# Optimization experiments

Hardware: AMD Instinct MI355X
Metric: run time of the kernel (lower is better)

The kernel has to match this reference:

```python
import jax, jax.numpy as jnp
import numpy as np

N, E, C, L, G, O = 100000, 1600000, 128, 7, 2, 40
BETA = 0.9
HEADS, HC = 1, 128  # heads=1, head_channels=hidden_channels=128


def setup_inputs() -> dict:
    key = jax.random.key(0)
    ks = jax.random.split(key, 16)
    s = 0.05  # ~ torch Linear init std for fan_in=128
    inp = {
        'x': jax.random.normal(ks[0], (N, C), jnp.float32),
        'edge_index': jax.random.randint(ks[1], (2, E), 0, N, jnp.int64),
        'Wh': jax.random.normal(ks[2], (L, C, C)) * s,
        'bh': jax.random.normal(ks[3], (L, C)) * s,
        'Wg': jax.random.normal(ks[4], (L, C, C)) * s,
        'bg': jax.random.normal(ks[5], (L, C)) * s,
        'Wl': jax.random.normal(ks[6], (L, C, C)) * s,
        'bl': jax.random.normal(ks[7], (L, C)) * s,
        'ln_g': jnp.ones((L, C)), 'ln_b': jnp.zeros((L, C)),
        'bn_g': jnp.ones((L, C)), 'bn_b': jnp.zeros((L, C)),
        'bn_rm': jnp.zeros((L, C)), 'bn_rv': jnp.ones((L, C)),
        'gWh': jax.random.normal(ks[8], (G, C, C)) * s,
        'gbh': jax.random.normal(ks[9], (G, C)) * s,
        'gWk': jax.random.normal(ks[10], (G, C, C)) * s,
        'gWv': jax.random.normal(ks[11], (G, C, C)) * s,
        'gln_g': jnp.ones((G, C)), 'gln_b': jnp.zeros((G, C)),
        'gWo': jax.random.normal(ks[12], (G, C, C)) * s,
        'gbo': jax.random.normal(ks[13], (G, C)) * s,
        'f_ln_g': jnp.ones((C,)), 'f_ln_b': jnp.zeros((C,)),
        'Wp': jax.random.normal(ks[14], (O, C)) * s,
        'bp': jax.random.normal(ks[15], (O,)) * s,
    }
    return inp


def _layer_norm(x, g, b, eps=1e-5):
    mu = jnp.mean(x, axis=-1, keepdims=True)
    var = jnp.mean((x - mu) ** 2, axis=-1, keepdims=True)
    return (x - mu) * jax.lax.rsqrt(var + eps) * g + b


def reference(x, edge_index, Wh, bh, Wg, bg, Wl, bl, ln_g, ln_b,
              bn_g, bn_b, bn_rm, bn_rv, gWh, gbh, gWk, gWv,
              gln_g, gln_b, gWo, gbo, f_ln_g, f_ln_b, Wp, bp):
    n = x.shape[0]
    src, dst = edge_index[0], edge_index[1]
    # gcn_norm with add_self_loops=True: deg over destination incl. self loop
    deg = jnp.zeros((n,), x.dtype).at[dst].add(1.0) + 1.0
    dinv = jax.lax.rsqrt(deg)
    enorm = (dinv[src] * dinv[dst])[:, None]   # [E,1]
    selfw = (dinv * dinv)[:, None]             # [N,1] self-loop weight

    x_local = jnp.zeros_like(x @ Wh[0].T)
    for i in range(L):
        h = jax.nn.relu(x @ Wh[i].T + bh[i])
        xw = x @ Wg[i].T                                  # GCN lin (bias separate)
        agg = jax.ops.segment_sum(xw[src] * enorm, dst, num_segments=n)
        conv = agg + xw * selfw + bg[i]
        x = conv + x @ Wl[i].T + bl[i]
        # BatchNorm1d in eval mode (running stats)
        x = (x - bn_rm[i]) * jax.lax.rsqrt(bn_rv[i] + 1e-5) * bn_g[i] + bn_b[i]
        x = jax.nn.relu(x)
        x = (1.0 - BETA) * _layer_norm(h * x, ln_g[i], ln_b[i]) + BETA * x
        x_local = x_local + x

    # global linear attention (PolynormerAttention, qk_shared=True, qkv_bias=False)
    xg = _layer_norm(x_local, f_ln_g, f_ln_b)
    for j in range(G):
        h = xg @ gWh[j].T + gbh[j]
        k = jax.nn.sigmoid(xg @ gWk[j].T).reshape(n, HEADS, HC)
        q = k
        v = (xg @ gWv[j].T).reshape(n, HEADS, HC)
        kv = jnp.einsum('ndh,ndm->dhm', k, v)            # [heads,hc,hc]
        num = jnp.einsum('ndh,dhm->ndm', q, kv)          # [N,heads,hc]
        k_sum = jnp.sum(k, axis=0)                       # [heads,hc]
        den = jnp.einsum('ndh,dh->nd', q, k_sum)[..., None]
        attn = (num / (den + 1e-6)).reshape(n, HEADS * HC)
        xg = _layer_norm(attn, gln_g[j], gln_b[j]) * (h + BETA)
        xg = jax.nn.relu(xg @ gWo[j].T + gbo[j])

    return xg @ Wp.T + bp
```

## Files before the change

### kernel.cpp

```cpp
#include <hip/hip_runtime.h>

typedef unsigned short u16;
typedef unsigned int u32;
typedef __attribute__((ext_vector_type(8))) short short8;
typedef __attribute__((ext_vector_type(8))) unsigned short ushort8v;
typedef __attribute__((ext_vector_type(4))) float f32x4;

#define CDIM 128

__device__ __forceinline__ float b2f(u16 u){ return __uint_as_float(((unsigned)u)<<16); }
__device__ __forceinline__ u16 f2b(float f){
  unsigned x = __float_as_uint(f);
  unsigned r = (x + 0x7fffu + ((x>>16)&1u)) >> 16;
  return (u16)r;
}
__device__ __forceinline__ float wsum64(float v){
  #pragma unroll
  for(int d=1; d<64; d<<=1) v += __shfl_xor(v, d, 64);
  return v;
}
__device__ __forceinline__ float wsum16(float v){
  v += __shfl_xor(v, 1, 64);
  v += __shfl_xor(v, 2, 64);
  v += __shfl_xor(v, 4, 64);
  v += __shfl_xor(v, 8, 64);
  return v;
}

__global__ void k_probe(const u32* __restrict__ x, const u32* __restrict__ ei, int* __restrict__ flags){
  __shared__ int s_bf, s_nz;
  if(threadIdx.x == 0){ s_bf = 0; s_nz = 0; }
  __syncthreads();
  int c_bf = 0, c_nz = 0;
  for(int i = threadIdx.x; i < 4096; i += 256){
    u32 w = x[i];
    u32 e = (w >> 7) & 0xFFu;
    if(e >= 100u && e <= 140u) c_bf++;
    if(ei[2*i + 1] != 0u) c_nz++;
  }
  atomicAdd(&s_bf, c_bf);
  atomicAdd(&s_nz, c_nz);
  __syncthreads();
  if(threadIdx.x == 0){
    flags[0] = (s_bf < 2048) ? 1 : 0;
    flags[1] = (s_nz < 8) ? 1 : 0;
  }
}

__global__ void k_cvt_x(const void* __restrict__ src, u16* __restrict__ dst, int n,
                        const int* __restrict__ flags){
  int i = (blockIdx.x*256 + threadIdx.x)*8;
  if(i + 7 >= n) return;
  if(flags[0]){
    const float* s = (const float*)src + i;
    float4 a = *(const float4*)s;
    float4 b = *(const float4*)(s + 4);
    ushort8v o;
    o[0]=f2b(a.x); o[1]=f2b(a.y); o[2]=f2b(a.z); o[3]=f2b(a.w);
    o[4]=f2b(b.x); o[5]=f2b(b.y); o[6]=f2b(b.z); o[7]=f2b(b.w);
    *(ushort8v*)(dst + i) = o;
  } else {
    *(ushort8v*)(dst + i) = *(const ushort8v*)((const u16*)src + i);
  }
}

struct CvtArgs {
  const void* src[24];
  u16* dst[24];
  int n[24];
};

__global__ void k_cvt_params(CvtArgs a, const int* __restrict__ flags){
  int seg = blockIdx.y;
  int i = blockIdx.x*256 + threadIdx.x;
  int n = a.n[seg];
  if(i >= n) return;
  if(flags[0]) a.dst[seg][i] = f2b(((const float*)a.src[seg])[i]);
  else         a.dst[seg][i] = ((const u16*)a.src[seg])[i];
}

__global__ void k_cvt_ei_count(const int* __restrict__ src, int* __restrict__ dst, int E,
                               const int* __restrict__ flags, u32* __restrict__ cnt){
  int i = blockIdx.x*256 + threadIdx.x;
  if(i >= 2*E) return;
  int v = flags[1] ? src[2*i] : src[i];
  dst[i] = v;
  if(i >= E) atomicAdd(&cnt[v], 1u);
}

__global__ __launch_bounds__(256) void k_scan1(const u32* __restrict__ cnt, int n, u32* __restrict__ bsum){
  const int lane = threadIdx.x & 63;
  const int wv = threadIdx.x >> 6;
  int i = blockIdx.x*256 + threadIdx.x;
  u32 v = (i < n) ? cnt[i] : 0u;
  #pragma unroll
  for(int d=1; d<64; d<<=1) v += (u32)__shfl_xor((int)v, d, 64);
  __shared__ u32 ws[4];
  if(lane == 0) ws[wv] = v;
  __syncthreads();
  if(threadIdx.x == 0) bsum[blockIdx.x] = ws[0] + ws[1] + ws[2] + ws[3];
}

__global__ __launch_bounds__(1024) void k_scan2(const u32* __restrict__ bsum, int nb, u32* __restrict__ bpre){
  __shared__ u32 s[1024];
  int t = threadIdx.x;
  u32 v = (t < nb) ? bsum[t] : 0u;
  s[t] = v;
  __syncthreads();
  for(int d=1; d<1024; d<<=1){
    u32 y = (t >= d) ? s[t-d] : 0u;
    __syncthreads();
    s[t] += y;
    __syncthreads();
  }
  if(t < nb) bpre[t] = s[t] - v;
}

__global__ __launch_bounds__(256) void k_scan3(const u32* __restrict__ cnt, int n,
                                               const u32* __restrict__ bpre,
                                               u32* __restrict__ rowstart, u32* __restrict__ cursor,
                                               float* __restrict__ dinv){
  const int lane = threadIdx.x & 63;
  const int wv = threadIdx.x >> 6;
  int i = blockIdx.x*256 + threadIdx.x;
  u32 v = (i < n) ? cnt[i] : 0u;
  u32 x = v;
  #pragma unroll
  for(int d=1; d<64; d<<=1){
    u32 y = (u32)__shfl_up((int)x, d, 64);
    if(lane >= d) x += y;
  }
  __shared__ u32 ws[4];
  if(lane == 63) ws[wv] = x;
  __syncthreads();
  u32 woff = 0;
  #pragma unroll
  for(int w=0; w<4; w++) if(w < wv) woff += ws[w];
  u32 incl = x + woff;
  u32 rs = bpre[blockIdx.x] + incl - v;
  if(i < n){
    rowstart[i] = rs;
    cursor[i] = rs;
    dinv[i] = rsqrtf((float)(v + 1u));
    if(i == n-1) rowstart[n] = rs + v;
  }
}

__global__ __launch_bounds__(256) void k_scatter8(
  const int* __restrict__ ei, int E, int Nn, int nsl,
  u32* __restrict__ cursor, const float* __restrict__ dinv, int2* __restrict__ colw)
{
  const int r = blockIdx.x & 7;
  const int slice = blockIdx.x >> 3;
  const int q = (Nn + 7) >> 3;
  const int lo = r*q;
  const int hi = (lo + q < Nn) ? lo + q : Nn;
  const int chunk = (E + nsl - 1) / nsl;
  int e0 = slice*chunk;
  int e1 = e0 + chunk; if(e1 > E) e1 = E;
  for(int e = e0 + threadIdx.x; e < e1; e += 256){
    int d = ei[E + e];
    if(d >= lo && d < hi){
      int s = ei[e];
      u32 p = atomicAdd(&cursor[d], 1u);
      colw[p] = make_int2(s, __float_as_int(dinv[s]));
    }
  }
}

__global__ __launch_bounds__(256) void k_gemm3(
  const u16* __restrict__ A, int M,
  const u16* __restrict__ W0, const u16* __restrict__ bs0, int op0, u16* __restrict__ O0,
  const u16* __restrict__ W1, const u16* __restrict__ bs1, int op1, u16* __restrict__ O1,
  const u16* __restrict__ W2, const u16* __restrict__ bs2, int op2, u16* __restrict__ O2)
{
  __shared__ u16 stg[4][32*136];
  const int lane = threadIdx.x & 63;
  const int wv = threadIdx.x >> 6;
  const int l16 = lane & 15, quad = lane >> 4;
  const long nbase = (long)blockIdx.x*128 + wv*32;

  const u16* Ws[3] = {W0, W1, W2};
  const u16* Bs[3] = {bs0, bs1, bs2};
  u16* Os[3] = {O0, O1, O2};
  const int ops[3] = {op0, op1, op2};
  const int w = blockIdx.y;
  const u16* Wm = Ws[w];
  const int op = ops[w];
  u16* Op = Os[w];
  const u16* bp = Bs[w];
  u16* st = stg[wv];

  short8 xf[2][4];
  #pragma unroll
  for(int nt=0; nt<2; nt++){
    long r = nbase + nt*16 + l16; if(r >= M) r = M-1;
    const u16* ap = A + r*CDIM + quad*8;
    #pragma unroll
    for(int kt=0; kt<4; kt++)
      xf[nt][kt] = *(const short8*)(ap + kt*32);
  }

  #pragma unroll
  for(int ct=0; ct<8; ct++){
    f32x4 acc0 = {0.f,0.f,0.f,0.f}, acc1 = {0.f,0.f,0.f,0.f};
    const u16* wp = Wm + (ct*16 + l16)*CDIM + quad*8;
    #pragma unroll
    for(int kt=0; kt<4; kt++){
      short8 wf = *(const short8*)(wp + kt*32);
      acc0 = __builtin_amdgcn_mfma_f32_16x16x32_bf16(wf, xf[0][kt], acc0, 0, 0, 0);
      acc1 = __builtin_amdgcn_mfma_f32_16x16x32_bf16(wf, xf[1][kt], acc1, 0, 0, 0);
    }
    float bv[4] = {0.f,0.f,0.f,0.f};
    if(bp){
      ushort4 bq = *(const ushort4*)(bp + ct*16 + quad*4);
      bv[0]=b2f(bq.x); bv[1]=b2f(bq.y); bv[2]=b2f(bq.z); bv[3]=b2f(bq.w);
    }
    #pragma unroll
    for(int nt=0; nt<2; nt++){
      f32x4 a = nt ? acc1 : acc0;
      u16 o[4];
      #pragma unroll
      for(int g=0; g<4; g++){
        float v = a[g] + bv[g];
        if(op == 1) v = fmaxf(v, 0.f);
        else if(op == 2) v = 1.f/(1.f + __expf(-v));
        o[g] = f2b(v);
      }
      u32 p0 = (u32)o[0] | ((u32)o[1] << 16);
      u32 p1 = (u32)o[2] | ((u32)o[3] << 16);
      *(uint2*)&st[(nt*16 + l16)*136 + ct*16 + quad*4] = make_uint2(p0, p1);
    }
  }
  #pragma unroll
  for(int p2=0; p2<8; p2++){
    int row = (p2>>2)*16 + (lane>>2);
    int seg = (lane&3) + (p2&3)*4;
    long node = nbase + row;
    ushort8v v = *(const ushort8v*)&st[row*136 + seg*8];
    if(node < M)
      *(ushort8v*)(Op + (size_t)node*CDIM + seg*8) = v;
  }
}

__global__ __launch_bounds__(256) void k_layer_epi(
  const u16* __restrict__ xw, const u16* __restrict__ h, const u16* __restrict__ xl,
  const int2* __restrict__ colw, const u32* __restrict__ rowstart, const float* __restrict__ dinv,
  const u16* __restrict__ bg, const u16* __restrict__ bng, const u16* __restrict__ bnb,
  const u16* __restrict__ bnrm, const u16* __restrict__ bnrv,
  const u16* __restrict__ lng, const u16* __restrict__ lnb,
  const u16* __restrict__ flng, const u16* __restrict__ flnb,
  float* __restrict__ xlocal, u16* __restrict__ xout, int n, int first, int final)
{
  __shared__ float redis[4][128];
  const int lane = threadIdx.x & 63;
  const int quad = lane >> 4;
  const int l16 = lane & 15;
  const int wv = threadIdx.x >> 6;
  int node = blockIdx.x*4 + wv;
  const int valid = (node < n);
  if(!valid) node = n - 1;
  const int cg = l16*8;
  u32 j0 = rowstart[node], j1 = rowstart[node+1];
  float a[8];
  #pragma unroll
  for(int g=0; g<8; g++) a[g] = 0.f;

  for(u32 base = j0; base < j1; base += 64){
    int avail = (int)(j1 - base);
    int cnt = avail < 64 ? avail : 64;
    int2 pw = make_int2(0, 0);
    if(lane < cnt) pw = colw[base + lane];
    int cntp = (cnt + 15) & ~15;
    for(int t = 0; t < cntp; t += 16){
      int s[4]; float w[4]; ushort8v v[4];
      #pragma unroll
      for(int u=0; u<4; u++){
        s[u] = __shfl(pw.x, t + u*4 + quad, 64);
        w[u] = __int_as_float(__shfl(pw.y, t + u*4 + quad, 64));
      }
      #pragma unroll
      for(int u=0; u<4; u++) v[u] = *(const ushort8v*)(xw + (size_t)s[u]*CDIM + cg);
      #pragma unroll
      for(int u=0; u<4; u++){
        #pragma unroll
        for(int g=0; g<8; g++) a[g] = fmaf(w[u], b2f(v[u][g]), a[g]);
      }
    }
  }
  #pragma unroll
  for(int g=0; g<8; g++){
    a[g] += __shfl_xor(a[g], 16, 64);
    a[g] += __shfl_xor(a[g], 32, 64);
  }
  if(quad == 0){
    *(float4*)&redis[wv][cg]     = make_float4(a[0],a[1],a[2],a[3]);
    *(float4*)&redis[wv][cg + 4] = make_float4(a[4],a[5],a[6],a[7]);
  }
  __syncthreads();
  const int c0 = lane*2;
  float2 av = *(float2*)&redis[wv][c0];
  float a0 = av.x, a1 = av.y;

  float dn = dinv[node], sw = dn*dn;
  size_t base = (size_t)node*CDIM + c0;
  ushort2 xwv = *(const ushort2*)(xw + base);
  ushort2 xlv = *(const ushort2*)(xl + base);
  ushort2 hv  = *(const ushort2*)(h  + base);
  float x10 = a0*dn + b2f(xwv.x)*sw + b2f(bg[c0])   + b2f(xlv.x);
  float x11 = a1*dn + b2f(xwv.y)*sw + b2f(bg[c0+1]) + b2f(xlv.y);
  float s0 = rsqrtf(b2f(bnrv[c0])   + 1e-5f) * b2f(bng[c0]);
  float s1 = rsqrtf(b2f(bnrv[c0+1]) + 1e-5f) * b2f(bng[c0+1]);
  float x20 = (x10 - b2f(bnrm[c0]))*s0   + b2f(bnb[c0]);
  float x21 = (x11 - b2f(bnrm[c0+1]))*s1 + b2f(bnb[c0+1]);
  float x30 = fmaxf(x20, 0.f);
  float x31 = fmaxf(x21, 0.f);
  float t0 = b2f(hv.x)*x30, t1 = b2f(hv.y)*x31;
  float mu = wsum64(t0 + t1) * (1.f/128.f);
  float d0 = t0 - mu, d1 = t1 - mu;
  float var = wsum64(d0*d0 + d1*d1) * (1.f/128.f);
  float inv = rsqrtf(var + 1e-5f);
  float y0 = d0*inv*b2f(lng[c0])   + b2f(lnb[c0]);
  float y1 = d1*inv*b2f(lng[c0+1]) + b2f(lnb[c0+1]);
  float xn0 = 0.1f*y0 + 0.9f*x30;
  float xn1 = 0.1f*y1 + 0.9f*x31;
  float2 xl2;
  if(first){
    xl2.x = xn0; xl2.y = xn1;
  } else {
    xl2 = *(float2*)(xlocal + base);
    xl2.x += xn0; xl2.y += xn1;
  }
  if(!final){
    if(valid){
      *(float2*)(xlocal + base) = xl2;
      ushort2 o; o.x = f2b(xn0); o.y = f2b(xn1);
      *(ushort2*)(xout + base) = o;
    }
  } else {
    float mu2 = wsum64(xl2.x + xl2.y) * (1.f/128.f);
    float e0 = xl2.x - mu2, e1 = xl2.y - mu2;
    float var2 = wsum64(e0*e0 + e1*e1) * (1.f/128.f);
    float inv2 = rsqrtf(var2 + 1e-5f);
    if(valid){
      ushort2 o;
      o.x = f2b(e0*inv2*b2f(flng[c0])   + b2f(flnb[c0]));
      o.y = f2b(e1*inv2*b2f(flng[c0+1]) + b2f(flnb[c0+1]));
      *(ushort2*)(xout + base) = o;
    }
  }
}

__global__ __launch_bounds__(256) void k_kv(
  const u16* __restrict__ kk, const u16* __restrict__ vv, int n, int npb,
  float* __restrict__ part)
{
  __shared__ float sk[8][128];
  __shared__ float sv[8][128];
  const int tid = threadIdx.x;
  const int tr = tid >> 4, tc = tid & 15;
  float acc[8][8];
  #pragma unroll
  for(int i=0;i<8;i++){
    #pragma unroll
    for(int j=0;j<8;j++) acc[i][j] = 0.f;
  }
  float ks[8];
  #pragma unroll
  for(int i=0;i<8;i++) ks[i] = 0.f;
  int start = blockIdx.x * npb;
  int end = start + npb; if(end > n) end = n;
  const int lr = tid >> 5;
  const int lc = (tid & 31) * 4;
  for(int g0 = start; g0 < end; g0 += 8){
    int cnt = end - g0; if(cnt > 8) cnt = 8;
    __syncthreads();
    if(lr < cnt){
      ushort4 kq = *(const ushort4*)(kk + (size_t)(g0+lr)*CDIM + lc);
      ushort4 vq = *(const ushort4*)(vv + (size_t)(g0+lr)*CDIM + lc);
      sk[lr][lc] = b2f(kq.x); sk[lr][lc+1] = b2f(kq.y); sk[lr][lc+2] = b2f(kq.z); sk[lr][lc+3] = b2f(kq.w);
      sv[lr][lc] = b2f(vq.x); sv[lr][lc+1] = b2f(vq.y); sv[lr][lc+2] = b2f(vq.z); sv[lr][lc+3] = b2f(vq.w);
    }
    __syncthreads();
    for(int r=0; r<cnt; r++){
      float4 ka = *(const float4*)&sk[r][tr*8];
      float4 kb = *(const float4*)&sk[r][tr*8+4];
      float4 va = *(const float4*)&sv[r][tc*8];
      float4 vb = *(const float4*)&sv[r][tc*8+4];
      float kr[8] = {ka.x,ka.y,ka.z,ka.w,kb.x,kb.y,kb.z,kb.w};
      float vr[8] = {va.x,va.y,va.z,va.w,vb.x,vb.y,vb.z,vb.w};
      #pragma unroll
      for(int i=0;i<8;i++){
        #pragma unroll
        for(int j=0;j<8;j++) acc[i][j] = fmaf(kr[i], vr[j], acc[i][j]);
      }
      if(tc == 0){
        #pragma unroll
        for(int i=0;i<8;i++) ks[i] += kr[i];
      }
    }
  }
  float* p = part + (size_t)blockIdx.x * 16512;
  #pragma unroll
  for(int i=0;i<8;i++){
    #pragma unroll
    for(int j=0;j<8;j++)
      p[(size_t)(tc*8+j)*CDIM + tr*8 + i] = acc[i][j];
  }
  if(tc == 0){
    #pragma unroll
    for(int i=0;i<8;i++) p[16384 + tr*8 + i] = ks[i];
  }
}

__global__ void k_kvred(const float* __restrict__ part, int nb, u16* __restrict__ Bext){
  int i = blockIdx.x*256 + threadIdx.x;
  if(i >= 144*128) return;
  float s = 0.f;
  if(i < 16512){
    #pragma unroll 8
    for(int b=0;b<nb;b++) s += part[(size_t)b*16512 + i];
  }
  Bext[i] = f2b(s);
}

__global__ __launch_bounds__(256) void k_attn(
  const u16* __restrict__ q, const u16* __restrict__ Bext, const u16* __restrict__ hg,
  const u16* __restrict__ g, const u16* __restrict__ b,
  u16* __restrict__ out, int M)
{
  __shared__ u16 stg[4][32*136];
  const int lane = threadIdx.x & 63;
  const int wv = threadIdx.x >> 6;
  const int l16 = lane & 15, quad = lane >> 4;
  const long rbase = (long)blockIdx.x*128 + wv*32;
  u16* st = stg[wv];

  short8 af[2][4];
  #pragma unroll
  for(int rt=0; rt<2; rt++){
    long r = rbase + rt*16 + l16; if(r >= M) r = M-1;
    const u16* ap = q + r*CDIM + quad*8;
    #pragma unroll
    for(int kt=0; kt<4; kt++)
      af[rt][kt] = *(const short8*)(ap + kt*32);
  }
  f32x4 acc[2][9];
  f32x4 zero = {0.f,0.f,0.f,0.f};
  #pragma unroll
  for(int rt=0; rt<2; rt++){
    #pragma unroll
    for(int ct=0; ct<9; ct++) acc[rt][ct] = zero;
  }
  #pragma unroll
  for(int ct=0; ct<9; ct++){
    const u16* wp = Bext + (ct*16 + l16)*CDIM + quad*8;
    #pragma unroll
    for(int kt=0; kt<4; kt++){
      short8 bf = *(const short8*)(wp + kt*32);
      acc[0][ct] = __builtin_amdgcn_mfma_f32_16x16x32_bf16(af[0][kt], bf, acc[0][ct], 0, 0, 0);
      acc[1][ct] = __builtin_amdgcn_mfma_f32_16x16x32_bf16(af[1][kt], bf, acc[1][ct], 0, 0, 0);
    }
  }
  #pragma unroll
  for(int rt=0; rt<2; rt++){
    float rden[4];
    #pragma unroll
    for(int gi=0; gi<4; gi++){
      float dv = __shfl(acc[rt][8][gi], lane & 48, 64);
      rden[gi] = 1.f/(dv + 1e-6f);
    }
    #pragma unroll
    for(int gi=0; gi<4; gi++){
      float sum = 0.f;
      #pragma unroll
      for(int ct=0; ct<8; ct++) sum += acc[rt][ct][gi]*rden[gi];
      float mu = wsum16(sum) * (1.f/128.f);
      float vs = 0.f;
      #pragma unroll
      for(int ct=0; ct<8; ct++){ float d = acc[rt][ct][gi]*rden[gi] - mu; vs = fmaf(d, d, vs); }
      float inv = rsqrtf(wsum16(vs)*(1.f/128.f) + 1e-5f);
      const int rowl = rt*16 + quad*4 + gi;
      #pragma unroll
      for(int ct=0; ct<8; ct++){
        int col = ct*16 + l16;
        float y = (acc[rt][ct][gi]*rden[gi] - mu)*inv*b2f(g[col]) + b2f(b[col]);
        st[rowl*136 + col] = f2b(y);
      }
    }
  }
  #pragma unroll
  for(int p2=0; p2<8; p2++){
    int row = (p2>>2)*16 + (lane>>2);
    int seg = (lane&3) + (p2&3)*4;
    long node = rbase + row;
    if(node >= M) node = M-1;
    ushort8v yv = *(const ushort8v*)&st[row*136 + seg*8];
    ushort8v hv = *(const ushort8v*)(hg + (size_t)node*CDIM + seg*8);
    ushort8v o;
    #pragma unroll
    for(int i2=0; i2<8; i2++)
      o[i2] = f2b(b2f(yv[i2]) * (b2f(hv[i2]) + 0.9f));
    if(rbase + row < M)
      *(ushort8v*)(out + (size_t)node*CDIM + seg*8) = o;
  }
}

__global__ __launch_bounds__(256) void k_gout(
  const u16* __restrict__ A, const u16* __restrict__ W, const u16* __restrict__ bs,
  void* __restrict__ outv, int M, const int* __restrict__ flags)
{
  const int lane = threadIdx.x & 63;
  const int wv = threadIdx.x >> 6;
  const int l16 = lane & 15, quad = lane >> 4;
  const long rbase = (long)blockIdx.x*128 + wv*32;
  const int f32m = flags[0];
  short8 af[2][4];
  #pragma unroll
  for(int rt=0; rt<2; rt++){
    long r = rbase + rt*16 + l16; if(r >= M) r = M-1;
    const u16* ap = A + r*CDIM + quad*8;
    #pragma unroll
    for(int kt=0; kt<4; kt++)
      af[rt][kt] = *(const short8*)(ap + kt*32);
  }
  f32x4 acc[2][3];
  f32x4 zero = {0.f,0.f,0.f,0.f};
  #pragma unroll
  for(int rt=0; rt<2; rt++){
    #pragma unroll
    for(int ct=0; ct<3; ct++) acc[rt][ct] = zero;
  }
  #pragma unroll
  for(int ct=0; ct<3; ct++){
    int row = ct*16 + l16; if(row > 39) row = 39;
    const u16* wp = W + row*CDIM + quad*8;
    #pragma unroll
    for(int kt=0; kt<4; kt++){
      short8 bf = *(const short8*)(wp + kt*32);
      acc[0][ct] = __builtin_amdgcn_mfma_f32_16x16x32_bf16(af[0][kt], bf, acc[0][ct], 0, 0, 0);
      acc[1][ct] = __builtin_amdgcn_mfma_f32_16x16x32_bf16(af[1][kt], bf, acc[1][ct], 0, 0, 0);
    }
  }
  #pragma unroll
  for(int ct=0; ct<3; ct++){
    int col = ct*16 + l16;
    if(col < 40){
      float bias = b2f(bs[col]);
      #pragma unroll
      for(int rt=0; rt<2; rt++){
        #pragma unroll
        for(int gi=0; gi<4; gi++){
          long r = rbase + rt*16 + quad*4 + gi;
          if(r < M){
            float v = acc[rt][ct][gi] + bias;
            if(f32m) ((float*)outv)[r*40 + col] = v;
            else     ((u16*)outv)[r*40 + col] = f2b(v);
          }
        }
      }
    }
  }
}

extern "C" void kernel_launch(void* const* d_in, const int* in_sizes, int n_in,
                              void* d_out, int out_size, void* d_ws, size_t ws_size,
                              hipStream_t stream)
{
  (void)n_in;
  const int C = CDIM;
  const int Nn = in_sizes[0] / C;
  const int E  = in_sizes[1] / 2;

  char* ws = (char*)d_ws;
  size_t off = 0;
  auto alloc = [&](size_t bytes) -> char* {
    char* p = ws + off;
    off = (off + bytes + 255) & ~(size_t)255;
    return p;
  };
  u16*   x_cur  = (u16*)  alloc((size_t)Nn*C*2);
  float* xlocal = (float*)alloc((size_t)Nn*C*4);
  u16*   hb     = (u16*)  alloc((size_t)Nn*C*2);
  u16*   xwb    = (u16*)  alloc((size_t)Nn*C*2);
  u16*   xlb    = (u16*)  alloc((size_t)Nn*C*2);
  float* dinv   = (float*)alloc((size_t)Nn*4);
  u32*   cnt    = (u32*)  alloc((size_t)Nn*4);
  u32*   rowst  = (u32*)  alloc((size_t)(Nn+1)*4);
  u32*   cursor = (u32*)  alloc((size_t)Nn*4);
  int2*  colw   = (int2*) alloc((size_t)E*8);
  u16*   Bext   = (u16*)  alloc((size_t)144*128*2);
  int*   flags  = (int*)  alloc(256);
  u32*   bsum   = (u32*)  alloc(1024*4);
  u32*   bpre   = (u32*)  alloc(1024*4);
  size_t ptot = 0;
  for(int k=2;k<26;k++) ptot += (size_t)in_sizes[k];
  u16* pbuf = (u16*)alloc(ptot*2);

  if(off > ws_size){
    hipMemsetAsync(d_out, 0, (size_t)out_size*2, stream);
    return;
  }

  const u16* pp[26];
  {
    size_t po = 0;
    for(int k=2;k<26;k++){ pp[k] = pbuf + po; po += (size_t)in_sizes[k]; }
  }
  const u16* cWh  = pp[2];  const u16* cbh  = pp[3];
  const u16* cWg  = pp[4];  const u16* cbg  = pp[5];
  const u16* cWl  = pp[6];  const u16* cbl  = pp[7];
  const u16* clng = pp[8];  const u16* clnb = pp[9];
  const u16* cbng = pp[10]; const u16* cbnb = pp[11];
  const u16* cbnrm= pp[12]; const u16* cbnrv= pp[13];
  const u16* cgWh = pp[14]; const u16* cgbh = pp[15];
  const u16* cgWk = pp[16]; const u16* cgWv = pp[17];
  const u16* cglng= pp[18]; const u16* cglnb= pp[19];
  const u16* cgWo = pp[20]; const u16* cgbo = pp[21];
  const u16* cflng= pp[22]; const u16* cflnb= pp[23];
  const u16* cWp  = pp[24]; const u16* cbp  = pp[25];

  u16* xb  = (u16*)xlocal;
  int* eib = (int*)((char*)xlocal + (size_t)Nn*C*2);
  u16* xg  = x_cur;
  float* kvpart = xlocal;

  const int NB_KV = 512;
  const int npb = (Nn + NB_KV - 1) / NB_KV;
  const int gblk = (Nn + 127) / 128;
  const int nodeblk = (Nn + 3) / 4;
  const int nscan = (Nn + 255) / 256;
  const int NSL = 512;

  k_probe<<<1, 256, 0, stream>>>((const u32*)d_in[0], (const u32*)d_in[1], flags);
  hipMemsetAsync(cnt, 0, (size_t)Nn*4, stream);
  k_cvt_ei_count<<<(2*E + 255)/256, 256, 0, stream>>>((const int*)d_in[1], eib, E, flags, cnt);
  k_cvt_x<<<(Nn*C/8 + 255)/256, 256, 0, stream>>>(d_in[0], xb, Nn*C, flags);
  {
    CvtArgs a;
    int maxn = 0;
    for(int k=2;k<26;k++){
      a.src[k-2] = d_in[k];
      a.dst[k-2] = (u16*)pp[k];
      a.n[k-2]   = in_sizes[k];
      if(in_sizes[k] > maxn) maxn = in_sizes[k];
    }
    dim3 g((maxn + 255)/256, 24);
    k_cvt_params<<<g, 256, 0, stream>>>(a, flags);
  }

  k_scan1<<<nscan, 256, 0, stream>>>(cnt, Nn, bsum);
  k_scan2<<<1, 1024, 0, stream>>>(bsum, nscan, bpre);
  k_scan3<<<nscan, 256, 0, stream>>>(cnt, Nn, bpre, rowst, cursor, dinv);
  k_scatter8<<<NSL*8, 256, 0, stream>>>(eib, E, Nn, NSL, cursor, dinv, colw);

  const u16* xa = xb;
  for(int i=0; i<7; i++){
    k_gemm3<<<dim3(gblk,3), 256, 0, stream>>>(xa, Nn,
        cWh + (size_t)i*C*C, cbh + (size_t)i*C, 1, hb,
        cWg + (size_t)i*C*C, (const u16*)nullptr, 0, xwb,
        cWl + (size_t)i*C*C, cbl + (size_t)i*C, 0, xlb);
    k_layer_epi<<<nodeblk, 256, 0, stream>>>(xwb, hb, xlb, colw, rowst, dinv,
        cbg + (size_t)i*C, cbng + (size_t)i*C, cbnb + (size_t)i*C,
        cbnrm + (size_t)i*C, cbnrv + (size_t)i*C,
        clng + (size_t)i*C, clnb + (size_t)i*C,
        cflng, cflnb,
        xlocal, x_cur, Nn, (i==0) ? 1 : 0, (i==6) ? 1 : 0);
    xa = x_cur;
  }

  for(int j=0; j<2; j++){
    k_gemm3<<<dim3(gblk,3), 256, 0, stream>>>(xg, Nn,
        cgWh + (size_t)j*C*C, cgbh + (size_t)j*C, 0, hb,
        cgWk + (size_t)j*C*C, (const u16*)nullptr, 2, xwb,
        cgWv + (size_t)j*C*C, (const u16*)nullptr, 0, xlb);
    k_kv   <<<NB_KV, 256, 0, stream>>>(xwb, xlb, Nn, npb, kvpart);
    k_kvred<<<(144*128 + 255)/256, 256, 0, stream>>>(kvpart, NB_KV, Bext);
    k_attn <<<gblk, 256, 0, stream>>>(xwb, Bext, hb, cglng + (size_t)j*C, cglnb + (size_t)j*C, xlb, Nn);
    k_gemm3<<<dim3(gblk,1), 256, 0, stream>>>(xlb, Nn,
        cgWo + (size_t)j*C*C, cgbo + (size_t)j*C, 1, xg,
        (const u16*)nullptr, (const u16*)nullptr, 0, (u16*)nullptr,
        (const u16*)nullptr, (const u16*)nullptr, 0, (u16*)nullptr);
  }

  k_gout<<<gblk, 256, 0, stream>>>(xg, cWp, cbp, d_out, Nn, flags);
}
```

Before: 1.720 ms.

## Fuse output projection and final head into attention kernel; drop gemm LDS staging

The global-attention kernel now applies the gWo projection with ReLU directly on its LDS-staged tile, and on the last global layer also computes the final Wp projection. This removes a separate gemm launch per global layer and the final output kernel, along with their intermediate HBM round trips. Separately, k_gemm3 writes MFMA results straight to global memory as 8-byte stores instead of staging through shared memory. That saves LDS traffic but produces less coalesced writes.

Measured after the change: 1.697 ms. About the same (-1.3%).

```diff
diff --git a/kernel.cpp b/kernel.cpp
--- a/kernel.cpp
+++ b/kernel.cpp
@@ -174,7 +174,6 @@
   const u16* __restrict__ W1, const u16* __restrict__ bs1, int op1, u16* __restrict__ O1,
   const u16* __restrict__ W2, const u16* __restrict__ bs2, int op2, u16* __restrict__ O2)
 {
-  __shared__ u16 stg[4][32*136];
   const int lane = threadIdx.x & 63;
   const int wv = threadIdx.x >> 6;
   const int l16 = lane & 15, quad = lane >> 4;
@@ -189,7 +188,6 @@
   const int op = ops[w];
   u16* Op = Os[w];
   const u16* bp = Bs[w];
-  u16* st = stg[wv];
 
   short8 xf[2][4];
   #pragma unroll
@@ -218,28 +216,22 @@
     }
     #pragma unroll
     for(int nt=0; nt<2; nt++){
-      f32x4 a = nt ? acc1 : acc0;
-      u16 o[4];
-      #pragma unroll
-      for(int g=0; g<4; g++){
-        float v = a[g] + bv[g];
-        if(op == 1) v = fmaxf(v, 0.f);
-        else if(op == 2) v = 1.f/(1.f + __expf(-v));
-        o[g] = f2b(v);
-      }
-      u32 p0 = (u32)o[0] | ((u32)o[1] << 16);
-      u32 p1 = (u32)o[2] | ((u32)o[3] << 16);
-      *(uint2*)&st[(nt*16 + l16)*136 + ct*16 + quad*4] = make_uint2(p0, p1);
-    }
-  }
-  #pragma unroll
-  for(int p2=0; p2<8; p2++){
-    int row = (p2>>2)*16 + (lane>>2);
-    int seg = (lane&3) + (p2&3)*4;
-    long node = nbase + row;
-    ushort8v v = *(const ushort8v*)&st[row*136 + seg*8];
-    if(node < M)
-      *(ushort8v*)(Op + (size_t)node*CDIM + seg*8) = v;
+      long node = nbase + nt*16 + l16;
+      if(node < M){
+        f32x4 a = nt ? acc1 : acc0;
+        u16 o[4];
+        #pragma unroll
+        for(int g=0; g<4; g++){
+          float v = a[g] + bv[g];
+          if(op == 1) v = fmaxf(v, 0.f);
+          else if(op == 2) v = 1.f/(1.f + __expf(-v));
+          o[g] = f2b(v);
+        }
+        u32 p0 = (u32)o[0] | ((u32)o[1] << 16);
+        u32 p1 = (u32)o[2] | ((u32)o[3] << 16);
+        *(uint2*)(Op + (size_t)node*CDIM + ct*16 + quad*4) = make_uint2(p0, p1);
+      }
+    }
   }
 }
 
@@ -427,7 +419,10 @@
 __global__ __launch_bounds__(256) void k_attn(
   const u16* __restrict__ q, const u16* __restrict__ Bext, const u16* __restrict__ hg,
   const u16* __restrict__ g, const u16* __restrict__ b,
-  u16* __restrict__ out, int M)
+  const u16* __restrict__ Wo, const u16* __restrict__ bo,
+  const u16* __restrict__ Wp, const u16* __restrict__ bp,
+  u16* __restrict__ xgout, void* __restrict__ outv,
+  int M, int last, const int* __restrict__ flags)
 {
   __shared__ u16 stg[4][32*136];
   const int lane = threadIdx.x & 63;
@@ -436,56 +431,58 @@
   const long rbase = (long)blockIdx.x*128 + wv*32;
   u16* st = stg[wv];
 
-  short8 af[2][4];
-  #pragma unroll
-  for(int rt=0; rt<2; rt++){
-    long r = rbase + rt*16 + l16; if(r >= M) r = M-1;
-    const u16* ap = q + r*CDIM + quad*8;
-    #pragma unroll
-    for(int kt=0; kt<4; kt++)
-      af[rt][kt] = *(const short8*)(ap + kt*32);
-  }
-  f32x4 acc[2][9];
-  f32x4 zero = {0.f,0.f,0.f,0.f};
-  #pragma unroll
-  for(int rt=0; rt<2; rt++){
-    #pragma unroll
-    for(int ct=0; ct<9; ct++) acc[rt][ct] = zero;
-  }
-  #pragma unroll
-  for(int ct=0; ct<9; ct++){
-    const u16* wp = Bext + (ct*16 + l16)*CDIM + quad*8;
-    #pragma unroll
-    for(int kt=0; kt<4; kt++){
-      short8 bf = *(const short8*)(wp + kt*32);
-      acc[0][ct] = __builtin_amdgcn_mfma_f32_16x16x32_bf16(af[0][kt], bf, acc[0][ct], 0, 0, 0);
-      acc[1][ct] = __builtin_amdgcn_mfma_f32_16x16x32_bf16(af[1][kt], bf, acc[1][ct], 0, 0, 0);
-    }
-  }
-  #pragma unroll
-  for(int rt=0; rt<2; rt++){
-    float rden[4];
-    #pragma unroll
-    for(int gi=0; gi<4; gi++){
-      float dv = __shfl(acc[rt][8][gi], lane & 48, 64);
-      rden[gi] = 1.f/(dv + 1e-6f);
-    }
-    #pragma unroll
-    for(int gi=0; gi<4; gi++){
-      float sum = 0.f;
-      #pragma unroll
-      for(int ct=0; ct<8; ct++) sum += acc[rt][ct][gi]*rden[gi];
-      float mu = wsum16(sum) * (1.f/128.f);
-      float vs = 0.f;
-      #pragma unroll
-      for(int ct=0; ct<8; ct++){ float d = acc[rt][ct][gi]*rden[gi] - mu; vs = fmaf(d, d, vs); }
-      float inv = rsqrtf(wsum16(vs)*(1.f/128.f) + 1e-5f);
-      const int rowl = rt*16 + quad*4 + gi;
-      #pragma unroll
-      for(int ct=0; ct<8; ct++){
-        int col = ct*16 + l16;
-        float y = (acc[rt][ct][gi]*rden[gi] - mu)*inv*b2f(g[col]) + b2f(b[col]);
-        st[rowl*136 + col] = f2b(y);
+  {
+    short8 af[2][4];
+    #pragma unroll
+    for(int rt=0; rt<2; rt++){
+      long r = rbase + rt*16 + l16; if(r >= M) r = M-1;
+      const u16* ap = q + r*CDIM + quad*8;
+      #pragma unroll
+      for(int kt=0; kt<4; kt++)
+        af[rt][kt] = *(const short8*)(ap + kt*32);
+    }
+    f32x4 acc[2][9];
+    f32x4 zero = {0.f,0.f,0.f,0.f};
+    #pragma unroll
+    for(int rt=0; rt<2; rt++){
+      #pragma unroll
+      for(int ct=0; ct<9; ct++) acc[rt][ct] = zero;
+    }
+    #pragma unroll
+    for(int ct=0; ct<9; ct++){
+      const u16* wp = Bext + (ct*16 + l16)*CDIM + quad*8;
+      #pragma unroll
+      for(int kt=0; kt<4; kt++){
+        short8 bf = *(const short8*)(wp + kt*32);
+        acc[0][ct] = __builtin_amdgcn_mfma_f32_16x16x32_bf16(af[0][kt], bf, acc[0][ct], 0, 0, 0);
+        acc[1][ct] = __builtin_amdgcn_mfma_f32_16x16x32_bf16(af[1][kt], bf, acc[1][ct], 0, 0, 0);
+      }
+    }
+    #pragma unroll
+    for(int rt=0; rt<2; rt++){
+      float rden[4];
+      #pragma unroll
+      for(int gi=0; gi<4; gi++){
+        float dv = __shfl(acc[rt][8][gi], lane & 48, 64);
+        rden[gi] = 1.f/(dv + 1e-6f);
+      }
+      #pragma unroll
+      for(int gi=0; gi<4; gi++){
+        float sum = 0.f;
+        #pragma unroll
+        for(int ct=0; ct<8; ct++) sum += acc[rt][ct][gi]*rden[gi];
+        float mu = wsum16(sum) * (1.f/128.f);
+        float vs = 0.f;
+        #pragma unroll
+        for(int ct=0; ct<8; ct++){ float d = acc[rt][ct][gi]*rden[gi] - mu; vs = fmaf(d, d, vs); }
+        float inv = rsqrtf(wsum16(vs)*(1.f/128.f) + 1e-5f);
+        const int rowl = rt*16 + quad*4 + gi;
+        #pragma unroll
+        for(int ct=0; ct<8; ct++){
+          int col = ct*16 + l16;
+          float y = (acc[rt][ct][gi]*rden[gi] - mu)*inv*b2f(g[col]) + b2f(b[col]);
+          st[rowl*136 + col] = f2b(y);
+        }
       }
     }
   }
@@ -501,61 +498,90 @@
     #pragma unroll
     for(int i2=0; i2<8; i2++)
       o[i2] = f2b(b2f(yv[i2]) * (b2f(hv[i2]) + 0.9f));
-    if(rbase + row < M)
-      *(ushort8v*)(out + (size_t)node*CDIM + seg*8) = o;
-  }
-}
-
-__global__ __launch_bounds__(256) void k_gout(
-  const u16* __restrict__ A, const u16* __restrict__ W, const u16* __restrict__ bs,
-  void* __restrict__ outv, int M, const int* __restrict__ flags)
-{
-  const int lane = threadIdx.x & 63;
-  const int wv = threadIdx.x >> 6;
-  const int l16 = lane & 15, quad = lane >> 4;
-  const long rbase = (long)blockIdx.x*128 + wv*32;
-  const int f32m = flags[0];
-  short8 af[2][4];
-  #pragma unroll
-  for(int rt=0; rt<2; rt++){
-    long r = rbase + rt*16 + l16; if(r >= M) r = M-1;
-    const u16* ap = A + r*CDIM + quad*8;
+    *(ushort8v*)&st[row*136 + seg*8] = o;
+  }
+  short8 pf[2][4];
+  #pragma unroll
+  for(int nt=0; nt<2; nt++){
     #pragma unroll
     for(int kt=0; kt<4; kt++)
-      af[rt][kt] = *(const short8*)(ap + kt*32);
-  }
-  f32x4 acc[2][3];
-  f32x4 zero = {0.f,0.f,0.f,0.f};
-  #pragma unroll
-  for(int rt=0; rt<2; rt++){
-    #pragma unroll
-    for(int ct=0; ct<3; ct++) acc[rt][ct] = zero;
-  }
-  #pragma unroll
-  for(int ct=0; ct<3; ct++){
-    int row = ct*16 + l16; if(row > 39) row = 39;
-    const u16* wp = W + row*CDIM + quad*8;
+      pf[nt][kt] = *(const short8*)&st[(nt*16 + l16)*136 + quad*8 + kt*32];
+  }
+  #pragma unroll
+  for(int ct=0; ct<8; ct++){
+    f32x4 a0 = {0.f,0.f,0.f,0.f}, a1 = {0.f,0.f,0.f,0.f};
+    const u16* wp = Wo + (ct*16 + l16)*CDIM + quad*8;
     #pragma unroll
     for(int kt=0; kt<4; kt++){
-      short8 bf = *(const short8*)(wp + kt*32);
-      acc[0][ct] = __builtin_amdgcn_mfma_f32_16x16x32_bf16(af[0][kt], bf, acc[0][ct], 0, 0, 0);
-      acc[1][ct] = __builtin_amdgcn_mfma_f32_16x16x32_bf16(af[1][kt], bf, acc[1][ct], 0, 0, 0);
-    }
-  }
-  #pragma unroll
-  for(int ct=0; ct<3; ct++){
-    int col = ct*16 + l16;
-    if(col < 40){
-      float bias = b2f(bs[col]);
-      #pragma unroll
-      for(int rt=0; rt<2; rt++){
+      short8 wf = *(const short8*)(wp + kt*32);
+      a0 = __builtin_amdgcn_mfma_f32_16x16x32_bf16(wf, pf[0][kt], a0, 0, 0, 0);
+      a1 = __builtin_amdgcn_mfma_f32_16x16x32_bf16(wf, pf[1][kt], a1, 0, 0, 0);
+    }
+    ushort4 bq = *(const ushort4*)(bo + ct*16 + quad*4);
+    float bv[4] = {b2f(bq.x), b2f(bq.y), b2f(bq.z), b2f(bq.w)};
+    #pragma unroll
+    for(int nt=0; nt<2; nt++){
+      f32x4 a = nt ? a1 : a0;
+      u16 o[4];
+      #pragma unroll
+      for(int g2=0; g2<4; g2++)
+        o[g2] = f2b(fmaxf(a[g2] + bv[g2], 0.f));
+      u32 p0 = (u32)o[0] | ((u32)o[1] << 16);
+      u32 p1 = (u32)o[2] | ((u32)o[3] << 16);
+      *(uint2*)&st[(nt*16 + l16)*136 + ct*16 + quad*4] = make_uint2(p0, p1);
+    }
+  }
+  if(!last){
+    #pragma unroll
+    for(int p2=0; p2<8; p2++){
+      int row = (p2>>2)*16 + (lane>>2);
+      int seg = (lane&3) + (p2&3)*4;
+      long node = rbase + row;
+      ushort8v v = *(const ushort8v*)&st[row*136 + seg*8];
+      if(node < M)
+        *(ushort8v*)(xgout + (size_t)node*CDIM + seg*8) = v;
+    }
+  } else {
+    const int f32m = flags[0];
+    short8 pf2[2][4];
+    #pragma unroll
+    for(int nt=0; nt<2; nt++){
+      #pragma unroll
+      for(int kt=0; kt<4; kt++)
+        pf2[nt][kt] = *(const short8*)&st[(nt*16 + l16)*136 + quad*8 + kt*32];
+    }
+    #pragma unroll
+    for(int ct=0; ct<3; ct++){
+      f32x4 a0 = {0.f,0.f,0.f,0.f}, a1 = {0.f,0.f,0.f,0.f};
+      int wrow = ct*16 + l16; if(wrow > 39) wrow = 39;
+      const u16* wp = Wp + wrow*CDIM + quad*8;
+      #pragma unroll
+      for(int kt=0; kt<4; kt++){
+        short8 wf = *(const short8*)(wp + kt*32);
+        a0 = __builtin_amdgcn_mfma_f32_16x16x32_bf16(wf, pf2[0][kt], a0, 0, 0, 0);
+        a1 = __builtin_amdgcn_mfma_f32_16x16x32_bf16(wf, pf2[1][kt], a1, 0, 0, 0);
+      }
+      const int ch0 = ct*16 + quad*4;
+      if(ch0 < 40){
+        ushort4 bq = *(const ushort4*)(bp + ch0);
+        float bv[4] = {b2f(bq.x), b2f(bq.y), b2f(bq.z), b2f(bq.w)};
         #pragma unroll
-        for(int gi=0; gi<4; gi++){
-          long r = rbase + rt*16 + quad*4 + gi;
-          if(r < M){
-            float v = acc[rt][ct][gi] + bias;
-            if(f32m) ((float*)outv)[r*40 + col] = v;
-            else     ((u16*)outv)[r*40 + col] = f2b(v);
+        for(int nt=0; nt<2; nt++){
+          long node = rbase + nt*16 + l16;
+          if(node < M){
+            f32x4 a = nt ? a1 : a0;
+            if(f32m){
+              float* op = (float*)outv + node*40 + ch0;
+              #pragma unroll
+              for(int g2=0; g2<4; g2++) op[g2] = a[g2] + bv[g2];
+            } else {
+              u16 o[4];
+              #pragma unroll
+              for(int g2=0; g2<4; g2++) o[g2] = f2b(a[g2] + bv[g2]);
+              u32 p0 = (u32)o[0] | ((u32)o[1] << 16);
+              u32 p1 = (u32)o[2] | ((u32)o[3] << 16);
+              *(uint2*)((u16*)outv + node*40 + ch0) = make_uint2(p0, p1);
+            }
           }
         }
       }
@@ -676,12 +702,9 @@
         cgWv + (size_t)j*C*C, (const u16*)nullptr, 0, xlb);
     k_kv   <<<NB_KV, 256, 0, stream>>>(xwb, xlb, Nn, npb, kvpart);
     k_kvred<<<(144*128 + 255)/256, 256, 0, stream>>>(kvpart, NB_KV, Bext);
-    k_attn <<<gblk, 256, 0, stream>>>(xwb, Bext, hb, cglng + (size_t)j*C, cglnb + (size_t)j*C, xlb, Nn);
-    k_gemm3<<<dim3(gblk,1), 256, 0, stream>>>(xlb, Nn,
-        cgWo + (size_t)j*C*C, cgbo + (size_t)j*C, 1, xg,
-        (const u16*)nullptr, (const u16*)nullptr, 0, (u16*)nullptr,
-        (const u16*)nullptr, (const u16*)nullptr, 0, (u16*)nullptr);
-  }
-
-  k_gout<<<gblk, 256, 0, stream>>>(xg, cWp, cbp, d_out, Nn, flags);
-}
+    k_attn <<<gblk, 256, 0, stream>>>(xwb, Bext, hb,
+        cglng + (size_t)j*C, cglnb + (size_t)j*C,
+        cgWo + (size_t)j*C*C, cgbo + (size_t)j*C,
+        cWp, cbp, xg, d_out, Nn, (j==1) ? 1 : 0, flags);
+  }
+}
```
